# Performance work log

Measured on AMD Instinct MI355X. Metric: run time of the kernel, lower is better.

The kernel has to match this reference:

```python
import jax, jax.numpy as jnp
import numpy as np

# E8P 12-bit-abs codebook construction (faithful vectorized port of the torch code)
_SHUF = np.array([0, 2, 1, 3, 4, 6, 5, 7])  # shuffle_map
# get_norm12() * 2 (the integer matrix before the /2)
_NORM12_X2 = np.array([
    [3, 1, 1, 1, 3, 3, 3, 3], [1, 3, 1, 1, 3, 3, 3, 3], [1, 1, 3, 1, 3, 3, 3, 3],
    [1, 1, 1, 3, 3, 3, 3, 3], [3, 3, 3, 1, 3, 3, 1, 1], [3, 3, 3, 1, 3, 1, 3, 1],
    [3, 3, 3, 1, 1, 3, 3, 1], [3, 3, 3, 1, 3, 1, 1, 3], [3, 3, 3, 1, 1, 3, 1, 3],
    [3, 3, 3, 1, 1, 1, 3, 3], [3, 3, 1, 3, 3, 3, 1, 1], [3, 3, 1, 3, 3, 1, 3, 1],
    [3, 3, 1, 3, 1, 3, 3, 1], [3, 3, 1, 3, 3, 1, 1, 3], [3, 3, 1, 3, 1, 3, 1, 3],
    [3, 3, 1, 3, 1, 1, 3, 3], [3, 1, 3, 3, 3, 3, 1, 1], [3, 1, 3, 3, 3, 1, 3, 1],
    [3, 1, 3, 3, 1, 3, 3, 1], [3, 1, 3, 3, 3, 1, 1, 3], [3, 1, 3, 3, 1, 3, 1, 3],
    [1, 3, 3, 3, 1, 1, 3, 3], [1, 3, 3, 3, 3, 3, 1, 1], [1, 3, 3, 3, 3, 1, 3, 1],
    [1, 3, 3, 3, 1, 3, 3, 1], [1, 3, 3, 3, 3, 1, 1, 3], [1, 3, 3, 3, 1, 3, 1, 3],
    [1, 1, 3, 3, 1, 3, 3, 3], [3, 3, 1, 1, 3, 3, 3, 1]], dtype=np.int64)


def _packed_abs_grid():
    # Enumerate D8+1/2 lattice points, working with doubled integer coords (odd ints in [-7,7])
    idx = np.arange(8 ** 8, dtype=np.int64)
    cols, s, nrm = [], 0, 0
    for i in range(8):  # torch.cartesian_prod order: first dim varies slowest
        v = (2 * (((idx >> (3 * (7 - i))) & 7) - 4) + 1).astype(np.int8)  # 2*x for x in {-3.5..3.5}
        cols.append(v)
        w = v.astype(np.int32)
        s = s + w
        nrm = nrm + w * w
    mask = (s % 4 == 0) & (nrm <= 40)
    V = np.stack([c[mask] for c in cols], axis=1)
    d8abs2 = np.unique(np.abs(V), axis=0).astype(np.int64)  # lexsorted, doubled abs values
    cba2 = np.concatenate([d8abs2, _NORM12_X2], axis=0)[:, _SHUF]  # doubled values (== 2*cba)
    parity = (cba2.sum(1) // 2) % 2  # == cba.sum(1) % 2
    col = cba2 * 2  # == cba * 4, integer byte values in [2,14]
    col[:, 7] = col[:, 7] * (1 - 2 * parity)
    acc = np.zeros(col.shape[0], dtype=np.int64)
    for i in range(8):
        acc = acc | (col[:, i] << (8 * i))
    assert acc.shape[0] == 256
    return acc


def _full_grid():
    # Decode all 2^16 codes into the [65536, 8] fp32 codebook (port of get_full_grid)
    acc = _packed_abs_grid()
    c = np.arange(1 << 16, dtype=np.int64)
    signs = c & 255
    p = signs ^ (signs >> 4)
    p ^= p >> 2
    p ^= p >> 1
    parity = p & 1  # xor of the 8 sign bits
    signs = signs ^ parity
    ac = acc[c >> 8]  # packed abs code per entry
    byt = ((ac[:, None] >> (8 * _SHUF)) & 255).astype(np.uint8).astype(np.int8).astype(np.float32) / 4.0
    neg = ((signs[:, None] >> (7 - _SHUF)) & 1).astype(bool)
    vals = np.where(neg, -byt, byt) + np.where(parity[:, None] == 1, np.float32(-0.25), np.float32(0.25))
    return vals.astype(np.float32)


def setup_inputs() -> dict:
    key = jax.random.key(0)
    k1, k2 = jax.random.split(key)
    B = 4096          # tokens (batch * seq)
    M = 4096          # out_features = Qidxs rows
    N = 512           # Qidxs cols; in_features = N * 8 = 4096
    inp = jax.random.normal(k1, (B, N * 8), dtype=jnp.float32)
    Qidxs = jax.random.randint(k2, (M, N), 0, 1 << 16, dtype=jnp.int32)
    grid = jnp.asarray(_full_grid())  # [65536, 8] fp32 decoded E8P codebook
    return {"input": inp, "Qidxs": Qidxs, "grid": grid}


def reference(input, Qidxs, grid):
    m, n = Qidxs.shape
    # Dequantize: each int16 code indexes an 8-vector of the E8P codebook
    W = jnp.take(grid, Qidxs, axis=0).reshape(m, n * 8)  # [m, n*8] decompressed weight
    return input @ W.T  # [B, m]
```

## Files before the change

kernel.cpp:

```cpp
#include <hip/hip_runtime.h>
#include <hip/hip_bf16.h>

#define B_DIM 4096
#define M_DIM 4096
#define K_DIM 4096
#define NCODE 512

typedef __attribute__((ext_vector_type(4))) float f32x4;
typedef __attribute__((ext_vector_type(8))) short short8;

__device__ __forceinline__ unsigned short f2bf(float f) {
    union { float f; unsigned u; } c; c.f = f;
    unsigned u = c.u;
    return (unsigned short)((u + 0x7FFFu + ((u >> 16) & 1u)) >> 16);
}

__global__ __launch_bounds__(256) void dequant_kernel(const int* __restrict__ Q,
                                                      const float* __restrict__ cb,
                                                      short* __restrict__ Wout) {
    const int t = blockIdx.x * 256 + threadIdx.x;
    const int code = Q[t] & 0xFFFF;
    const float4* g = (const float4*)(cb + (size_t)code * 8);
    const float4 v0 = g[0];
    const float4 v1 = g[1];
    short8 o;
    o[0] = f2bf(v0.x); o[1] = f2bf(v0.y); o[2] = f2bf(v0.z); o[3] = f2bf(v0.w);
    o[4] = f2bf(v1.x); o[5] = f2bf(v1.y); o[6] = f2bf(v1.z); o[7] = f2bf(v1.w);
    *(short8*)(Wout + (size_t)t * 8) = o;
}

__global__ __launch_bounds__(256) void cvt_kernel(const float* __restrict__ in,
                                                  short* __restrict__ outb) {
    const int t = blockIdx.x * 256 + threadIdx.x;
    const float4* p = (const float4*)(in + (size_t)t * 8);
    const float4 v0 = p[0];
    const float4 v1 = p[1];
    short8 o;
    o[0] = f2bf(v0.x); o[1] = f2bf(v0.y); o[2] = f2bf(v0.z); o[3] = f2bf(v0.w);
    o[4] = f2bf(v1.x); o[5] = f2bf(v1.y); o[6] = f2bf(v1.z); o[7] = f2bf(v1.w);
    *(short8*)(outb + (size_t)t * 8) = o;
}

#define BM 256
#define BN 256
#define BK 32
#define NT (K_DIM / BK)

#define GLD(src, dst) \
    __builtin_amdgcn_global_load_lds( \
        (const __attribute__((address_space(1))) void*)(src), \
        (__attribute__((address_space(3))) void*)(dst), 16, 0, 0)

__global__ __launch_bounds__(512, 2) void gemm_bt_kernel(const short* __restrict__ A,
                                                         const short* __restrict__ Wd,
                                                         float* __restrict__ C) {
    __shared__ short lds[4 * 16384];

    const int tid  = threadIdx.x;
    const int wave = tid >> 6;
    const int lane = tid & 63;

    const int bid = blockIdx.x;
    const int xcd = bid & 7;
    const int s   = bid >> 3;
    const int by  = (xcd >> 1) * 4 + (s >> 3);
    const int bx  = (xcd & 1) * 8 + (s & 7);

    const int rowBase = by * BM;
    const int colBase = bx * BN;

    const int wr = wave >> 2;
    const int wc = wave & 3;

    const int rA0 = tid >> 2;
    const int uu  = (tid & 3) ^ ((rA0 >> 1) & 3);
    const short* aSrc0 = A  + (size_t)(rowBase + rA0) * K_DIM + uu * 8;
    const short* aSrc1 = A  + (size_t)(rowBase + rA0 + 128) * K_DIM + uu * 8;
    const short* bSrc0 = Wd + (size_t)(colBase + rA0) * K_DIM + uu * 8;
    const short* bSrc1 = Wd + (size_t)(colBase + rA0 + 128) * K_DIM + uu * 8;

    const int l15 = lane & 15;
    const int l4  = lane >> 4;
    const int sx  = (l15 >> 1) & 3;
    const int aRd = (wr * 128 + l15) * 32 + (l4 ^ sx) * 8;
    const int bRd = 8192 + (wc * 64 + l15) * 32 + (l4 ^ sx) * 8;

    f32x4 acc[8][4] = {};

#pragma unroll
    for (int p = 0; p < 3; ++p) {
        const int koff = p * BK;
        short* base = &lds[p * 16384];
        GLD(aSrc0 + koff, base + wave * 512);
        GLD(aSrc1 + koff, base + 4096 + wave * 512);
        GLD(bSrc0 + koff, base + 8192 + wave * 512);
        GLD(bSrc1 + koff, base + 12288 + wave * 512);
    }
    asm volatile("s_waitcnt vmcnt(8)" ::: "memory");
    __builtin_amdgcn_s_barrier();

    for (int t = 0; t < NT; ++t) {
        const int buf    = (t & 3) * 16384;
        const int tpre   = (t + 3 < NT) ? (t + 3) : (NT - 1);
        const int kpre   = tpre * BK;
        const int bufpre = ((t + 3) & 3) * 16384;

        short8 af0[4], bf[4];
#pragma unroll
        for (int m = 0; m < 4; ++m)
            af0[m] = *(const short8*)&lds[buf + aRd + m * 512];
#pragma unroll
        for (int n = 0; n < 4; ++n)
            bf[n] = *(const short8*)&lds[buf + bRd + n * 512];
        GLD(aSrc0 + kpre, &lds[bufpre + wave * 512]);
        GLD(aSrc1 + kpre, &lds[bufpre + 4096 + wave * 512]);
        asm volatile("s_waitcnt vmcnt(6)" ::: "memory");
        __builtin_amdgcn_s_barrier();
        __builtin_amdgcn_s_setprio(1);
#pragma unroll
        for (int m = 0; m < 4; ++m)
#pragma unroll
            for (int n = 0; n < 4; ++n)
                acc[m][n] = __builtin_amdgcn_mfma_f32_16x16x32_bf16(
                    af0[m], bf[n], acc[m][n], 0, 0, 0);
        __builtin_amdgcn_s_setprio(0);
        __builtin_amdgcn_s_barrier();

        short8 af1[4];
#pragma unroll
        for (int m = 0; m < 4; ++m)
            af1[m] = *(const short8*)&lds[buf + aRd + (m + 4) * 512];
        GLD(bSrc0 + kpre, &lds[bufpre + 8192 + wave * 512]);
        GLD(bSrc1 + kpre, &lds[bufpre + 12288 + wave * 512]);
        __builtin_amdgcn_s_barrier();
        __builtin_amdgcn_s_setprio(1);
#pragma unroll
        for (int m = 0; m < 4; ++m)
#pragma unroll
            for (int n = 0; n < 4; ++n)
                acc[m + 4][n] = __builtin_amdgcn_mfma_f32_16x16x32_bf16(
                    af1[m], bf[n], acc[m + 4][n], 0, 0, 0);
        __builtin_amdgcn_s_setprio(0);
        __builtin_amdgcn_s_barrier();
    }

    const int r0 = rowBase + wr * 128 + l4 * 4;
    const int c0 = colBase + wc * 64 + l15;
#pragma unroll
    for (int m = 0; m < 8; ++m)
#pragma unroll
        for (int n = 0; n < 4; ++n) {
            float* cp = C + (size_t)(r0 + m * 16) * M_DIM + (c0 + n * 16);
#pragma unroll
            for (int reg = 0; reg < 4; ++reg)
                cp[(size_t)reg * M_DIM] = acc[m][n][reg];
        }
}

extern "C" void kernel_launch(void* const* d_in, const int* in_sizes, int n_in,
                              void* d_out, int out_size, void* d_ws, size_t ws_size,
                              hipStream_t stream) {
    const float* inp  = (const float*)d_in[0];
    const int*   qidx = (const int*)d_in[1];
    const float* cb   = (const float*)d_in[2];
    float* out = (float*)d_out;

    short* Wb = (short*)d_ws;
    short* Ab = Wb + (size_t)M_DIM * K_DIM;

    const int n_codes = M_DIM * NCODE;
    dequant_kernel<<<n_codes / 256, 256, 0, stream>>>(qidx, cb, Wb);

    const int n_cvt = B_DIM * K_DIM / 8;
    cvt_kernel<<<n_cvt / 256, 256, 0, stream>>>(inp, Ab);

    gemm_bt_kernel<<<256, 512, 0, stream>>>(Ab, Wb, out);
}
```

Measured before the change: 149.3 us.

## Double-buffer LDS fragment reads across GEMM iterations with ping-pong registers

Restructures the bf16 GEMM main loop so the next K-tile's A/B fragments are read from LDS into a second register set while the second half of the current tile's MFMAs run. The loop is unrolled by two, alternating two fragment register sets. Per-iteration barriers drop from four to two, and an explicit lgkmcnt wait is added. The aim is to hide LDS read latency behind MFMA work and cut synchronisation, at the cost of extra VGPRs under the 512-thread, 2-blocks-per-CU launch bound.

New measurement: 141.9 us. 1.05x faster.

```diff
diff --git a/kernel.cpp b/kernel.cpp
--- a/kernel.cpp
+++ b/kernel.cpp
@@ -51,6 +51,8 @@
         (const __attribute__((address_space(1))) void*)(src), \
         (__attribute__((address_space(3))) void*)(dst), 16, 0, 0)
 
+#define MFMA(a, b, c) __builtin_amdgcn_mfma_f32_16x16x32_bf16(a, b, c, 0, 0, 0)
+
 __global__ __launch_bounds__(512, 2) void gemm_bt_kernel(const short* __restrict__ A,
                                                          const short* __restrict__ Wd,
                                                          float* __restrict__ C) {
@@ -86,6 +88,7 @@
     const int bRd = 8192 + (wc * 64 + l15) * 32 + (l4 ^ sx) * 8;
 
     f32x4 acc[8][4] = {};
+    short8 aX[4], bX[4], aY[4], bY[4], a1[4];
 
 #pragma unroll
     for (int p = 0; p < 3; ++p) {
@@ -98,51 +101,56 @@
     }
     asm volatile("s_waitcnt vmcnt(8)" ::: "memory");
     __builtin_amdgcn_s_barrier();
+#pragma unroll
+    for (int m = 0; m < 4; ++m) aX[m] = *(const short8*)&lds[aRd + m * 512];
+#pragma unroll
+    for (int n = 0; n < 4; ++n) bX[n] = *(const short8*)&lds[bRd + n * 512];
 
-    for (int t = 0; t < NT; ++t) {
-        const int buf    = (t & 3) * 16384;
-        const int tpre   = (t + 3 < NT) ? (t + 3) : (NT - 1);
-        const int kpre   = tpre * BK;
-        const int bufpre = ((t + 3) & 3) * 16384;
+#define ITER_BODY(T, AC, BC, AN, BN)                                          \
+    {                                                                         \
+        const int buf    = ((T) & 3) * 16384;                                 \
+        const int bufn   = (((T) + 1) & 3) * 16384;                           \
+        const int tpre   = ((T) + 3 < NT) ? ((T) + 3) : (NT - 1);             \
+        const int kpre   = tpre * BK;                                         \
+        const int bufpre = (((T) + 3) & 3) * 16384;                           \
+        _Pragma("unroll")                                                     \
+        for (int m = 0; m < 4; ++m)                                           \
+            a1[m] = *(const short8*)&lds[buf + aRd + (m + 4) * 512];          \
+        GLD(aSrc0 + kpre, &lds[bufpre + wave * 512]);                         \
+        GLD(aSrc1 + kpre, &lds[bufpre + 4096 + wave * 512]);                  \
+        asm volatile("s_waitcnt vmcnt(6)" ::: "memory");                      \
+        __builtin_amdgcn_s_barrier();                                         \
+        __builtin_amdgcn_s_setprio(1);                                        \
+        _Pragma("unroll")                                                     \
+        for (int m = 0; m < 4; ++m)                                           \
+            _Pragma("unroll")                                                 \
+            for (int n = 0; n < 4; ++n)                                       \
+                acc[m][n] = MFMA(AC[m], BC[n], acc[m][n]);                    \
+        __builtin_amdgcn_s_setprio(0);                                        \
+        GLD(bSrc0 + kpre, &lds[bufpre + 8192 + wave * 512]);                  \
+        GLD(bSrc1 + kpre, &lds[bufpre + 12288 + wave * 512]);                 \
+        asm volatile("s_waitcnt lgkmcnt(0)" ::: "memory");                    \
+        __builtin_amdgcn_s_barrier();                                         \
+        _Pragma("unroll")                                                     \
+        for (int m = 0; m < 4; ++m)                                           \
+            AN[m] = *(const short8*)&lds[bufn + aRd + m * 512];               \
+        _Pragma("unroll")                                                     \
+        for (int n = 0; n < 4; ++n)                                           \
+            BN[n] = *(const short8*)&lds[bufn + bRd + n * 512];               \
+        __builtin_amdgcn_s_setprio(1);                                        \
+        _Pragma("unroll")                                                     \
+        for (int m = 0; m < 4; ++m)                                           \
+            _Pragma("unroll")                                                 \
+            for (int n = 0; n < 4; ++n)                                       \
+                acc[m + 4][n] = MFMA(a1[m], BC[n], acc[m + 4][n]);            \
+        __builtin_amdgcn_s_setprio(0);                                        \
+    }
 
-        short8 af0[4], bf[4];
-#pragma unroll
-        for (int m = 0; m < 4; ++m)
-            af0[m] = *(const short8*)&lds[buf + aRd + m * 512];
-#pragma unroll
-        for (int n = 0; n < 4; ++n)
-            bf[n] = *(const short8*)&lds[buf + bRd + n * 512];
-        GLD(aSrc0 + kpre, &lds[bufpre + wave * 512]);
-        GLD(aSrc1 + kpre, &lds[bufpre + 4096 + wave * 512]);
-        asm volatile("s_waitcnt vmcnt(6)" ::: "memory");
-        __builtin_amdgcn_s_barrier();
-        __builtin_amdgcn_s_setprio(1);
-#pragma unroll
-        for (int m = 0; m < 4; ++m)
-#pragma unroll
-            for (int n = 0; n < 4; ++n)
-                acc[m][n] = __builtin_amdgcn_mfma_f32_16x16x32_bf16(
-                    af0[m], bf[n], acc[m][n], 0, 0, 0);
-        __builtin_amdgcn_s_setprio(0);
-        __builtin_amdgcn_s_barrier();
-
-        short8 af1[4];
-#pragma unroll
-        for (int m = 0; m < 4; ++m)
-            af1[m] = *(const short8*)&lds[buf + aRd + (m + 4) * 512];
-        GLD(bSrc0 + kpre, &lds[bufpre + 8192 + wave * 512]);
-        GLD(bSrc1 + kpre, &lds[bufpre + 12288 + wave * 512]);
-        __builtin_amdgcn_s_barrier();
-        __builtin_amdgcn_s_setprio(1);
-#pragma unroll
-        for (int m = 0; m < 4; ++m)
-#pragma unroll
-            for (int n = 0; n < 4; ++n)
-                acc[m + 4][n] = __builtin_amdgcn_mfma_f32_16x16x32_bf16(
-                    af1[m], bf[n], acc[m + 4][n], 0, 0, 0);
-        __builtin_amdgcn_s_setprio(0);
-        __builtin_amdgcn_s_barrier();
+    for (int t2 = 0; t2 < NT; t2 += 2) {
+        ITER_BODY(t2,     aX, bX, aY, bY)
+        ITER_BODY(t2 + 1, aY, bY, aX, bX)
     }
+#undef ITER_BODY
 
     const int r0 = rowBase + wr * 128 + l4 * 4;
     const int c0 = colBase + wc * 64 + l15;
```
